# Performance work log

Hardware: AMD Instinct MI355X
Metric: run time of the kernel (lower is better)

Reference implementation:

```python
import jax, jax.numpy as jnp
import numpy as np

B = 1024   # batch
N = 8192   # code length (power of 2)
K = 4096   # info bits


def polar_transform(v):
    """Recursive XOR butterfly (polar encoding), vectorized.

    Faithful to the TF loop: at each stage every length-L block is split into
    positions 0::2 ('odd') and 1::2 ('even'); output block = [odd^even, even].
    v: (B, N, 1) int32 in {0,1}. Returns (B, N, 1).
    """
    b, n, _ = v.shape
    blocks, L = 1, n
    while L > 1:
        vv = v.reshape(b, blocks, L // 2, 2, 1)
        odd = vv[:, :, :, 0, :]   # in-block indices 0,2,4,...
        even = vv[:, :, :, 1, :]  # in-block indices 1,3,5,...
        xor = (odd + even) % 2    # tf.math.floormod(V_odd + V_even, 2)
        v = jnp.concatenate([xor, even], axis=2).reshape(b, blocks * L, 1)
        blocks *= 2
        L //= 2
    return v


def setup_inputs() -> dict:
    key = jax.random.key(0)
    k1, k2 = jax.random.split(key)
    # info bits as float 0/1 (kept float so the bwd variant has a float primal)
    info_bits = jnp.round(jax.random.uniform(k1, (B, K), dtype=jnp.float32))
    # hoisted tf.random.uniform(..., maxval=2, dtype=int32)
    u_random = jax.random.randint(k2, (B, N), 0, 2, dtype=jnp.int32)
    # info_set = sorted top-K entries of the reliability permutation
    perm = np.random.RandomState(0).permutation(N)
    info_set = jnp.asarray(np.sort(perm[:K]).astype(np.int32))
    return {"info_bits": info_bits, "u_random": u_random, "info_set": info_set}


def reference(info_bits, u_random, info_set):
    # scatter info bits into the random word at the info positions
    u2d = u_random.at[:, info_set].set(info_bits.astype(jnp.int32))
    # frozen-indicator word: info positions marked with 2
    f2d = u_random.at[:, info_set].set(2)
    u = u2d[..., None]          # (B, N, 1)
    f = f2d[..., None]          # (B, N, 1)
    x = polar_transform(u)      # (B, N, 1)
    r = jnp.stack((1 - u_random, u_random), axis=-1).astype(jnp.float32)  # (B,N,2)
    p = jnp.full((B, N, 2), 0.5, dtype=jnp.float32)
    return x, f, u, p, r
```

## Files before the change

kernel.cpp:

```cpp
#include <hip/hip_runtime.h>
#include <hip/hip_bf16.h>
#include <stdint.h>

#define BB 1024
#define NN 8192
#define KK 4096

__global__ void init_pos_kernel(int* __restrict__ pos) {
    int i = blockIdx.x * blockDim.x + threadIdx.x;
    if (i < NN) pos[i] = -1;
}
__global__ void scatter_pos_kernel(const int* __restrict__ info_set, int* __restrict__ pos) {
    int k = blockIdx.x * blockDim.x + threadIdx.x;
    if (k < KK) pos[info_set[k]] = k;
}

__global__ __launch_bounds__(256) void polar_main_kernel(
    const float* __restrict__ info_bits,
    const int*   __restrict__ u_random,
    const int*   __restrict__ pos,
    float*       __restrict__ out)
{
    __shared__ uint32_t yw[256];

    const int b    = blockIdx.x;
    const int t    = threadIdx.x;
    const int lane = t & 63;
    const int ww   = t >> 6;

    float*  x_out = out;
    float*  f_out = out + (size_t)BB * NN;
    float*  u_out = out + 2ull * BB * NN;
    float2* p_out = (float2*)(out + 3ull * BB * NN);
    float2* r_out = (float2*)(out + 5ull * BB * NN);

    const size_t rowb  = (size_t)b * NN;
    const int*   urow  = u_random + rowb;
    const float* ibrow = info_bits + (size_t)b * KK;

    const int base = ww * 2048;
    #pragma unroll 4
    for (int it = 0; it < 32; ++it) {
        const int idx = base + it * 64 + lane;
        const int ur  = urow[idx];
        const int k   = pos[idx];
        int uval, fval;
        if (k >= 0) { uval = (int)(ibrow[k] + 0.5f); fval = 2; }
        else        { uval = ur;                     fval = ur; }

        const size_t o = rowb + idx;
        u_out[o] = (float)uval;
        f_out[o] = (float)fval;
        p_out[o] = make_float2(0.5f, 0.5f);
        r_out[o] = make_float2((float)(1 - ur), (float)ur);

        unsigned long long m = __ballot(uval);
        if (lane == 0) {
            const int w0 = idx >> 5;
            yw[w0]     = (uint32_t)m;
            yw[w0 + 1] = (uint32_t)(m >> 32);
        }
    }
    __syncthreads();

    if (ww == 0) {
        uint32_t W0 = yw[lane];
        uint32_t W1 = yw[lane + 64];
        uint32_t W2 = yw[lane + 128];
        uint32_t W3 = yw[lane + 192];

        #define INWORD(W) \
            W ^= (W >> 1)  & 0x55555555u; \
            W ^= (W >> 2)  & 0x33333333u; \
            W ^= (W >> 4)  & 0x0F0F0F0Fu; \
            W ^= (W >> 8)  & 0x00FF00FFu; \
            W ^= (W >> 16) & 0x0000FFFFu;
        INWORD(W0) INWORD(W1) INWORD(W2) INWORD(W3)
        #undef INWORD

        #pragma unroll
        for (int wb = 0; wb < 6; ++wb) {
            const bool keep = ((lane >> wb) & 1);
            uint32_t p0 = (uint32_t)__shfl_xor((int)W0, 1 << wb);
            uint32_t p1 = (uint32_t)__shfl_xor((int)W1, 1 << wb);
            uint32_t p2 = (uint32_t)__shfl_xor((int)W2, 1 << wb);
            uint32_t p3 = (uint32_t)__shfl_xor((int)W3, 1 << wb);
            if (!keep) { W0 ^= p0; W1 ^= p1; W2 ^= p2; W3 ^= p3; }
        }

        W0 ^= W1; W2 ^= W3;
        W0 ^= W2; W1 ^= W3;

        yw[lane]       = W0;
        yw[lane + 64]  = W1;
        yw[lane + 128] = W2;
        yw[lane + 192] = W3;
    }
    __syncthreads();

    const uint32_t w = yw[__builtin_bitreverse32((uint32_t)t) >> 24];
    #pragma unroll
    for (int j = 0; j < 32; ++j) {
        const int sb = (int)(__builtin_bitreverse32((uint32_t)j) >> 27);
        x_out[rowb + t + 256 * j] = (float)((w >> sb) & 1u);
    }
}

extern "C" void kernel_launch(void* const* d_in, const int* in_sizes, int n_in,
                              void* d_out, int out_size, void* d_ws, size_t ws_size,
                              hipStream_t stream) {
    const float* info_bits = (const float*)d_in[0];
    const int*   u_random  = (const int*)  d_in[1];
    const int*   info_set  = (const int*)  d_in[2];
    float*       out       = (float*)d_out;
    int*         pos       = (int*)d_ws;

    init_pos_kernel<<<NN / 256, 256, 0, stream>>>(pos);
    scatter_pos_kernel<<<KK / 256, 256, 0, stream>>>(info_set, pos);
    polar_main_kernel<<<BB, 256, 0, stream>>>(info_bits, u_random, pos, out);
}
```

Before: 297.6 us.

## Vectorize polar kernel I/O with 16-byte nontemporal stores and 512-thread blocks

Each thread now loads u_random and the position map as int4 and writes every output tensor as float4 through nontemporal stores. This replaces the scalar and float2 stores. The ballot-based bit packing becomes a shuffle-based nibble packing with a new shared-word layout, and the x output is rebuilt with bit-reversed indexing to match that layout. Blocks grow to 512 threads with a launch-bounds occupancy hint. The goal is to cut memory instruction count and cache pollution on this write-heavy kernel, at the cost of a more intricate bit-index mapping that must stay exactly consistent.

```diff
diff --git a/kernel.cpp b/kernel.cpp
--- a/kernel.cpp
+++ b/kernel.cpp
@@ -5,6 +5,9 @@
 #define BB 1024
 #define NN 8192
 #define KK 4096
+
+typedef float vf4 __attribute__((ext_vector_type(4)));
+typedef int   vi4 __attribute__((ext_vector_type(4)));
 
 __global__ void init_pos_kernel(int* __restrict__ pos) {
     int i = blockIdx.x * blockDim.x + threadIdx.x;
@@ -15,7 +18,14 @@
     if (k < KK) pos[info_set[k]] = k;
 }
 
-__global__ __launch_bounds__(256) void polar_main_kernel(
+__device__ __forceinline__ void nt_store(vf4* p, vf4 v) {
+    __builtin_nontemporal_store(v, p);
+}
+__device__ __forceinline__ vf4 mk4(float a, float b, float c, float d) {
+    vf4 v; v.x = a; v.y = b; v.z = c; v.w = d; return v;
+}
+
+__global__ __launch_bounds__(512, 4) void polar_main_kernel(
     const float* __restrict__ info_bits,
     const int*   __restrict__ u_random,
     const int*   __restrict__ pos,
@@ -28,38 +38,44 @@
     const int lane = t & 63;
     const int ww   = t >> 6;
 
-    float*  x_out = out;
-    float*  f_out = out + (size_t)BB * NN;
-    float*  u_out = out + 2ull * BB * NN;
-    float2* p_out = (float2*)(out + 3ull * BB * NN);
-    float2* r_out = (float2*)(out + 5ull * BB * NN);
+    vf4* x4 = (vf4*)(out)                 + (size_t)b * (NN / 4);
+    vf4* f4 = (vf4*)(out + (size_t)BB*NN) + (size_t)b * (NN / 4);
+    vf4* u4 = (vf4*)(out + 2ull*BB*NN)    + (size_t)b * (NN / 4);
+    vf4* p4 = (vf4*)(out + 3ull*BB*NN)    + (size_t)b * (NN / 2);
+    vf4* r4 = (vf4*)(out + 5ull*BB*NN)    + (size_t)b * (NN / 2);
 
-    const size_t rowb  = (size_t)b * NN;
-    const int*   urow  = u_random + rowb;
+    const vi4*   ur4p  = (const vi4*)(u_random + (size_t)b * NN);
+    const vi4*   pos4p = (const vi4*)pos;
     const float* ibrow = info_bits + (size_t)b * KK;
 
-    const int base = ww * 2048;
-    #pragma unroll 4
-    for (int it = 0; it < 32; ++it) {
-        const int idx = base + it * 64 + lane;
-        const int ur  = urow[idx];
-        const int k   = pos[idx];
-        int uval, fval;
-        if (k >= 0) { uval = (int)(ibrow[k] + 0.5f); fval = 2; }
-        else        { uval = ur;                     fval = ur; }
+    #pragma unroll
+    for (int it = 0; it < 4; ++it) {
+        const int idx4 = it * 512 + t;
+        const vi4 ur = ur4p[idx4];
+        const vi4 kk = pos4p[idx4];
 
-        const size_t o = rowb + idx;
-        u_out[o] = (float)uval;
-        f_out[o] = (float)fval;
-        p_out[o] = make_float2(0.5f, 0.5f);
-        r_out[o] = make_float2((float)(1 - ur), (float)ur);
+        int u0 = ur.x, u1 = ur.y, u2 = ur.z, u3 = ur.w;
+        int f0 = u0,   f1 = u1,   f2 = u2,   f3 = u3;
+        if (kk.x >= 0) { u0 = ibrow[kk.x] > 0.5f; f0 = 2; }
+        if (kk.y >= 0) { u1 = ibrow[kk.y] > 0.5f; f1 = 2; }
+        if (kk.z >= 0) { u2 = ibrow[kk.z] > 0.5f; f2 = 2; }
+        if (kk.w >= 0) { u3 = ibrow[kk.w] > 0.5f; f3 = 2; }
 
-        unsigned long long m = __ballot(uval);
-        if (lane == 0) {
-            const int w0 = idx >> 5;
-            yw[w0]     = (uint32_t)m;
-            yw[w0 + 1] = (uint32_t)(m >> 32);
-        }
+        nt_store(&u4[idx4], mk4((float)u0, (float)u1, (float)u2, (float)u3));
+        nt_store(&f4[idx4], mk4((float)f0, (float)f1, (float)f2, (float)f3));
+        nt_store(&p4[idx4 * 2],     mk4(0.5f, 0.5f, 0.5f, 0.5f));
+        nt_store(&p4[idx4 * 2 + 1], mk4(0.5f, 0.5f, 0.5f, 0.5f));
+        nt_store(&r4[idx4 * 2],
+                 mk4((float)(1 - ur.x), (float)ur.x, (float)(1 - ur.y), (float)ur.y));
+        nt_store(&r4[idx4 * 2 + 1],
+                 mk4((float)(1 - ur.z), (float)ur.z, (float)(1 - ur.w), (float)ur.w));
+
+        uint32_t x = (uint32_t)(u0 | (u1 << 1) | (u2 << 2) | (u3 << 3));
+        x |= ((uint32_t)__shfl_xor((int)x, 1)) << 4;
+        x |= ((uint32_t)__shfl_xor((int)x, 2)) << 8;
+        x |= ((uint32_t)__shfl_xor((int)x, 4)) << 16;
+        if ((lane & 7) == 0)
+            yw[it * 64 + ww * 8 + (lane >> 3)] = x;
     }
     __syncthreads();
 
@@ -98,11 +114,17 @@
     }
     __syncthreads();
 
-    const uint32_t w = yw[__builtin_bitreverse32((uint32_t)t) >> 24];
     #pragma unroll
-    for (int j = 0; j < 32; ++j) {
-        const int sb = (int)(__builtin_bitreverse32((uint32_t)j) >> 27);
-        x_out[rowb + t + 256 * j] = (float)((w >> sb) & 1u);
+    for (int it = 0; it < 4; ++it) {
+        const int s = it * 512 + t;
+        const uint32_t q = __builtin_bitreverse32((uint32_t)s) >> 21;
+        const int w   = (int)(q >> 5);
+        const int bsh = (int)(q & 31u);
+        const float x0 = (float)((yw[w]       >> bsh) & 1u);
+        const float x1 = (float)((yw[w + 128] >> bsh) & 1u);
+        const float x2 = (float)((yw[w + 64]  >> bsh) & 1u);
+        const float x3 = (float)((yw[w + 192] >> bsh) & 1u);
+        nt_store(&x4[s], mk4(x0, x1, x2, x3));
     }
 }
 
@@ -117,5 +139,5 @@
 
     init_pos_kernel<<<NN / 256, 256, 0, stream>>>(pos);
     scatter_pos_kernel<<<KK / 256, 256, 0, stream>>>(info_set, pos);
-    polar_main_kernel<<<BB, 256, 0, stream>>>(info_bits, u_random, pos, out);
+    polar_main_kernel<<<BB, 512, 0, stream>>>(info_bits, u_random, pos, out);
 }
```

After: 290.0 us. 2.5% less time.
